# Kernel optimization log

Hardware: AMD Instinct MI355X
Metric: run time of the kernel (lower is better)

Reference implementation:

```python
import jax, jax.numpy as jnp
import numpy as np

N = 100000   # nodes
E = 800000   # edges
D = 128      # uniform hidden width
L = 3        # number of SAGE layers (len(hidden_channels)-1)
EPS = 1e-5   # BatchNorm eps


def setup_inputs() -> dict:
    key = jax.random.key(0)
    ks = jax.random.split(key, 7)
    s = 1.0 / np.sqrt(D)
    x = jax.random.normal(ks[0], (N, D), jnp.float32)
    edge_index = jax.random.randint(ks[1], (2, E), 0, N)
    Wl = jax.random.normal(ks[2], (L, D, D), jnp.float32) * s  # neighbor-branch weight (out,in)
    Wr = jax.random.normal(ks[3], (L, D, D), jnp.float32) * s  # root-branch weight (out,in)
    b = jax.random.normal(ks[4], (L, D), jnp.float32) * 0.01   # bias (lin_l only, PyG default)
    gamma = 1.0 + 0.1 * jax.random.normal(ks[5], (L, D), jnp.float32)
    beta = 0.1 * jax.random.normal(ks[6], (L, D), jnp.float32)
    return {"x": x, "edge_index": edge_index, "Wl": Wl, "Wr": Wr, "b": b,
            "gamma": gamma, "beta": beta}


def _sage(x, src, dst, Wl, Wr, b):
    # PyG SAGEConv: out = lin_l(mean_{j->i} x_j) + lin_r(x_i)
    agg = jax.ops.segment_sum(x[src], dst, num_segments=N)          # [N, D]
    cnt = jax.ops.segment_sum(jnp.ones((src.shape[0], 1), x.dtype), dst,
                              num_segments=N)                        # [N, 1]
    agg = agg / jnp.maximum(cnt, 1.0)  # mean; isolated nodes stay 0
    return agg @ Wl.T + x @ Wr.T + b


def _bn(x, g, be):
    # BatchNorm1d over the node axis, batch statistics, biased variance
    m = jnp.mean(x, axis=0)
    v = jnp.var(x, axis=0)
    return g * (x - m) * jax.lax.rsqrt(v + EPS) + be


def reference(x, edge_index, Wl, Wr, b, gamma, beta):
    src, dst = edge_index[0], edge_index[1]
    # hidden layers: SAGEConv -> ELU -> (dropout, eval no-op) -> BatchNorm
    for i in range(L - 1):
        h = jax.nn.elu(_sage(x, src, dst, Wl[i], Wr[i], b[i]))
        x = _bn(h, gamma[i], beta[i])
    # final layer: SAGEConv -> BatchNorm (no ELU/dropout)
    x = _bn(_sage(x, src, dst, Wl[L - 1], Wr[L - 1], b[L - 1]), gamma[L - 1], beta[L - 1])
    return x
```

## Files before the change

kernel.cpp:

```cpp
#include <hip/hip_runtime.h>
#include <hip/hip_bf16.h>

#define N_NODES 100000
#define N_EDGES 800000
#define DD 128
#define NBLK 1563
#define NSCAN1 391
#define EPSV 1e-5f

typedef short bf16x8 __attribute__((ext_vector_type(8)));
typedef short bf16x4 __attribute__((ext_vector_type(4)));
typedef float f32x4 __attribute__((ext_vector_type(4)));

__device__ __forceinline__ short f2bf(float f) {
    unsigned u = __float_as_uint(f);
    unsigned r = (u + 0x7fffu + ((u >> 16) & 1u)) >> 16;
    return (short)r;
}
__device__ __forceinline__ float bf2f(short s) {
    return __uint_as_float(((unsigned)(unsigned short)s) << 16);
}

__global__ void k_setup(const float* __restrict__ x, short* __restrict__ xbf,
                        const int* __restrict__ dst, int* __restrict__ cnt) {
    int i = blockIdx.x * 256 + threadIdx.x;
    if (i < N_NODES * DD / 8) {
        f32x4 v0 = *(const f32x4*)(x + (size_t)i * 8);
        f32x4 v1 = *(const f32x4*)(x + (size_t)i * 8 + 4);
        bf16x8 t;
        t[0] = f2bf(v0.x); t[1] = f2bf(v0.y); t[2] = f2bf(v0.z); t[3] = f2bf(v0.w);
        t[4] = f2bf(v1.x); t[5] = f2bf(v1.y); t[6] = f2bf(v1.z); t[7] = f2bf(v1.w);
        *(bf16x8*)&xbf[(size_t)i * 8] = t;
    }
    if (i < N_EDGES) atomicAdd(&cnt[dst[i]], 1);
}

__global__ void k_scan1(const int* __restrict__ cnt, int* __restrict__ off,
                        int* __restrict__ bsums) {
    __shared__ int s[256];
    int i = blockIdx.x * 256 + threadIdx.x;
    int t = threadIdx.x;
    s[t] = (i < N_NODES) ? cnt[i] : 0;
    __syncthreads();
    for (int d = 1; d < 256; d <<= 1) {
        int x = 0;
        if (t >= d) x = s[t - d];
        __syncthreads();
        s[t] += x;
        __syncthreads();
    }
    if (i < N_NODES) off[i + 1] = s[t];
    if (t == 255) bsums[blockIdx.x] = s[255];
}

__global__ void k_scan2(int* __restrict__ bsums) {
    __shared__ int s[512];
    int t = threadIdx.x;
    s[t] = (t < NSCAN1) ? bsums[t] : 0;
    __syncthreads();
    for (int d = 1; d < 512; d <<= 1) {
        int x = 0;
        if (t >= d) x = s[t - d];
        __syncthreads();
        s[t] += x;
        __syncthreads();
    }
    if (t < NSCAN1) bsums[t] = s[t];
}

__global__ void k_scan3(int* __restrict__ off, const int* __restrict__ bsums) {
    int i = blockIdx.x * 256 + threadIdx.x;
    int add = (blockIdx.x > 0) ? bsums[blockIdx.x - 1] : 0;
    if (i < N_NODES) off[i + 1] += add;
    if (i == 0) off[0] = 0;
}

__global__ void k_fill(const int* __restrict__ src, const int* __restrict__ dst,
                       const int* __restrict__ off, int* __restrict__ cur,
                       int* __restrict__ elist) {
    int e = blockIdx.x * 256 + threadIdx.x;
    if (e < N_EDGES) {
        int d = dst[e];
        int p = atomicSub(&cur[d], 1);
        elist[off[d] + p - 1] = src[e];
    }
}

__global__ void k_fold(const float* __restrict__ wl, const float* __restrict__ wr,
                       const float* __restrict__ b, const float* __restrict__ aff,
                       int use_aff,
                       short* __restrict__ wblo, short* __restrict__ wbro,
                       float* __restrict__ bias_base, float* __restrict__ bias_deg) {
    int o = blockIdx.x;
    int k = threadIdx.x;
    float a = use_aff ? aff[k] : 1.f;
    float c = use_aff ? aff[128 + k] : 0.f;
    float vl = wl[o * DD + k], vr = wr[o * DD + k];
    wblo[o * DD + k] = f2bf(vl * a);
    wbro[o * DD + k] = f2bf(vr * a);
    __shared__ float s1[128], s2[128];
    s1[k] = c * vr; s2[k] = c * vl;
    __syncthreads();
    for (int d = 64; d > 0; d >>= 1) {
        if (k < d) { s1[k] += s1[k + d]; s2[k] += s2[k + d]; }
        __syncthreads();
    }
    if (k == 0) {
        bias_base[o] = b[o] + s1[0];
        bias_deg[o] = s2[0];
    }
}

template <bool ELU_ON>
__global__ __launch_bounds__(512, 6) void k_sage(
    const short* __restrict__ xbf,
    const int* __restrict__ off, const int* __restrict__ elist,
    const short* __restrict__ wl, const short* __restrict__ wr,
    const float* __restrict__ bias_base, const float* __restrict__ bias_deg,
    short* __restrict__ hout, float* __restrict__ partials)
{
    __shared__ short agg_t[64 * 128];
    __shared__ int sdeg[64];
    __shared__ float sstat[8 * 128];
    const int tid = threadIdx.x;
    const int wu = __builtin_amdgcn_readfirstlane(tid >> 6);
    const int l = tid & 63;
    const int base = blockIdx.x * 64;
    const int qw = l >> 4;
    const int ll = l & 15;

    const int growb = (wu >> 1) * 16 + (wu & 1) * 8;
    for (int i = 0; i < 8; i += 2) {
        const int m0 = growb + i;
        const int m1 = m0 + 1;
        const int g0 = base + m0;
        const int g1 = base + m1;
        float A0[8], A1[8], B0[8], B1[8];
#pragma unroll
        for (int j = 0; j < 8; ++j) { A0[j] = A1[j] = B0[j] = B1[j] = 0.f; }
        int ea = 0, eA = 0, eb = 0, eB = 0;
        if (g0 < N_NODES) { ea = off[g0]; eA = off[g0 + 1]; }
        if (g1 < N_NODES) { eb = off[g1]; eB = off[g1 + 1]; }
        const int dA = eA - ea, dB = eB - eb;
        int e = ea + qw;
        int f = eb + qw;
        while (e + 4 < eA && f + 4 < eB) {
            int s0 = elist[e], s1 = elist[e + 4];
            int s2 = elist[f], s3 = elist[f + 4];
            bf16x8 v0 = *(const bf16x8*)(xbf + (size_t)s0 * DD + 8 * ll);
            bf16x8 v1 = *(const bf16x8*)(xbf + (size_t)s1 * DD + 8 * ll);
            bf16x8 v2 = *(const bf16x8*)(xbf + (size_t)s2 * DD + 8 * ll);
            bf16x8 v3 = *(const bf16x8*)(xbf + (size_t)s3 * DD + 8 * ll);
#pragma unroll
            for (int j = 0; j < 8; ++j) {
                A0[j] += bf2f(v0[j]); A1[j] += bf2f(v1[j]);
                B0[j] += bf2f(v2[j]); B1[j] += bf2f(v3[j]);
            }
            e += 8; f += 8;
        }
        while (e + 4 < eA) {
            int s0 = elist[e], s1 = elist[e + 4];
            bf16x8 v0 = *(const bf16x8*)(xbf + (size_t)s0 * DD + 8 * ll);
            bf16x8 v1 = *(const bf16x8*)(xbf + (size_t)s1 * DD + 8 * ll);
#pragma unroll
            for (int j = 0; j < 8; ++j) { A0[j] += bf2f(v0[j]); A1[j] += bf2f(v1[j]); }
            e += 8;
        }
        if (e < eA) {
            int s0 = elist[e];
            bf16x8 v0 = *(const bf16x8*)(xbf + (size_t)s0 * DD + 8 * ll);
#pragma unroll
            for (int j = 0; j < 8; ++j) A0[j] += bf2f(v0[j]);
        }
        while (f + 4 < eB) {
            int s2 = elist[f], s3 = elist[f + 4];
            bf16x8 v2 = *(const bf16x8*)(xbf + (size_t)s2 * DD + 8 * ll);
            bf16x8 v3 = *(const bf16x8*)(xbf + (size_t)s3 * DD + 8 * ll);
#pragma unroll
            for (int j = 0; j < 8; ++j) { B0[j] += bf2f(v2[j]); B1[j] += bf2f(v3[j]); }
            f += 8;
        }
        if (f < eB) {
            int s2 = elist[f];
            bf16x8 v2 = *(const bf16x8*)(xbf + (size_t)s2 * DD + 8 * ll);
#pragma unroll
            for (int j = 0; j < 8; ++j) B0[j] += bf2f(v2[j]);
        }
#pragma unroll
        for (int j = 0; j < 8; ++j) {
            float sA = A0[j] + A1[j];
            sA += __shfl_xor(sA, 16, 64);
            sA += __shfl_xor(sA, 32, 64);
            A0[j] = sA;
            float sB = B0[j] + B1[j];
            sB += __shfl_xor(sB, 16, 64);
            sB += __shfl_xor(sB, 32, 64);
            B0[j] = sB;
        }
        if (l == 0) { sdeg[m0] = dA; sdeg[m1] = dB; }
        if (qw == 0) {
            float invA = dA > 0 ? 1.f / (float)dA : 0.f;
            float invB = dB > 0 ? 1.f / (float)dB : 0.f;
            bf16x8 tA, tB;
#pragma unroll
            for (int j = 0; j < 8; ++j) { tA[j] = f2bf(A0[j] * invA); tB[j] = f2bf(B0[j] * invB); }
            *(bf16x8*)&agg_t[m0 * DD + ((8 * ll) ^ ((m0 & 7) << 3))] = tA;
            *(bf16x8*)&agg_t[m1 * DD + ((8 * ll) ^ ((m1 & 7) << 3))] = tB;
        }
    }
    __syncthreads();

    const int p = wu >> 1;
    const int half = wu & 1;
    f32x4 acc[4];
#pragma unroll
    for (int nb = 0; nb < 4; ++nb) acc[nb] = f32x4{0.f, 0.f, 0.f, 0.f};
    const int mrow = p * 16 + (l & 15);
    const int kg = (l >> 4) * 8;
    const int nloc = l & 15;
    const int groot = min(base + mrow, N_NODES - 1);
#pragma unroll
    for (int ks = 0; ks < 4; ++ks) {
        int kk = ks * 32 + kg;
        int sw = kk ^ ((mrow & 7) << 3);
        bf16x8 aa = *(const bf16x8*)&agg_t[mrow * DD + sw];
        bf16x8 ax = *(const bf16x8*)(xbf + (size_t)groot * DD + kk);
#pragma unroll
        for (int nb = 0; nb < 4; ++nb) {
            int n = half * 64 + nb * 16 + nloc;
            bf16x8 bl = *(const bf16x8*)&wl[n * DD + kk];
            bf16x8 br = *(const bf16x8*)&wr[n * DD + kk];
            acc[nb] = __builtin_amdgcn_mfma_f32_16x16x32_bf16(aa, bl, acc[nb], 0, 0, 0);
            acc[nb] = __builtin_amdgcn_mfma_f32_16x16x32_bf16(ax, br, acc[nb], 0, 0, 0);
        }
    }
    __syncthreads();

    int degf[4];
#pragma unroll
    for (int r = 0; r < 4; ++r) degf[r] = sdeg[p * 16 + (l >> 4) * 4 + r];

    float colS[4], colQ[4];
#pragma unroll
    for (int nb = 0; nb < 4; ++nb) {
        int n = half * 64 + nb * 16 + nloc;
        float bb = bias_base[n];
        float bd = bias_deg[n];
        float cs = 0.f, cq = 0.f;
#pragma unroll
        for (int r = 0; r < 4; ++r) {
            int m = p * 16 + (l >> 4) * 4 + r;
            int g = base + m;
            float hv = acc[nb][r] + bb + (degf[r] > 0 ? bd : 0.f);
            if (ELU_ON) hv = hv > 0.f ? hv : expm1f(hv);
            agg_t[m * DD + (n ^ ((m & 7) << 3))] = f2bf(hv);
            float hm = (g < N_NODES) ? hv : 0.f;
            cs += hm;
            cq += hm * hm;
        }
        colS[nb] = cs; colQ[nb] = cq;
    }
#pragma unroll
    for (int nb = 0; nb < 4; ++nb) {
        colS[nb] += __shfl_xor(colS[nb], 16, 64);
        colS[nb] += __shfl_xor(colS[nb], 32, 64);
        colQ[nb] += __shfl_xor(colQ[nb], 16, 64);
        colQ[nb] += __shfl_xor(colQ[nb], 32, 64);
    }
    if (l < 16) {
#pragma unroll
        for (int nb = 0; nb < 4; ++nb) {
            sstat[wu * 128 + nb * 16 + l]      = colS[nb];
            sstat[wu * 128 + 64 + nb * 16 + l] = colQ[nb];
        }
    }
    __syncthreads();

#pragma unroll
    for (int k = 0; k < 2; ++k) {
        int idx = (k * 512 + tid) * 8;
        int m = idx >> 7, c = idx & 127;
        int g = base + m;
        if (g < N_NODES) {
            bf16x8 v = *(const bf16x8*)&agg_t[m * DD + (c ^ ((m & 7) << 3))];
            *(bf16x8*)&hout[(size_t)g * DD + c] = v;
        }
    }
    if (tid < 256) {
        int f = tid & 127;
        int part = tid >> 7;
        int hsel = f >> 6;
        int cw = part * 64 + (f & 63);
        float v = 0.f;
#pragma unroll
        for (int pr = 0; pr < 4; ++pr) v += sstat[(2 * pr + hsel) * 128 + cw];
        partials[blockIdx.x * 256 + tid] = v;
    }
}

__global__ void k_reduce(const float* __restrict__ partials,
                         const float* __restrict__ gamma, const float* __restrict__ beta,
                         float* __restrict__ aff) {
    int f = blockIdx.x;
    int t = threadIdx.x;
    float s = 0.f, q = 0.f;
    for (int i = t; i < NBLK; i += 256) {
        s += partials[i * 256 + f];
        q += partials[i * 256 + 128 + f];
    }
    __shared__ float rs[256], rq[256];
    rs[t] = s; rq[t] = q;
    __syncthreads();
    for (int d = 128; d > 0; d >>= 1) {
        if (t < d) { rs[t] += rs[t + d]; rq[t] += rq[t + d]; }
        __syncthreads();
    }
    if (t == 0) {
        float mean = rs[0] / (float)N_NODES;
        float var = rq[0] / (float)N_NODES - mean * mean;
        float a = gamma[f] * rsqrtf(var + EPSV);
        aff[f] = a;
        aff[128 + f] = beta[f] - mean * a;
    }
}

__global__ void k_apply(const short* __restrict__ hin, const float* __restrict__ aff,
                        float* __restrict__ out) {
    int i = blockIdx.x * 256 + threadIdx.x;
    if (i < N_NODES * DD / 8) {
        bf16x8 v = *(const bf16x8*)(hin + (size_t)i * 8);
        int f = (i * 8) & 127;
        f32x4 a0 = *(const f32x4*)(aff + f);
        f32x4 a1 = *(const f32x4*)(aff + f + 4);
        f32x4 c0 = *(const f32x4*)(aff + 128 + f);
        f32x4 c1 = *(const f32x4*)(aff + 128 + f + 4);
        f32x4 o0, o1;
        o0.x = bf2f(v[0]) * a0.x + c0.x; o0.y = bf2f(v[1]) * a0.y + c0.y;
        o0.z = bf2f(v[2]) * a0.z + c0.z; o0.w = bf2f(v[3]) * a0.w + c0.w;
        o1.x = bf2f(v[4]) * a1.x + c1.x; o1.y = bf2f(v[5]) * a1.y + c1.y;
        o1.z = bf2f(v[6]) * a1.z + c1.z; o1.w = bf2f(v[7]) * a1.w + c1.w;
        *(f32x4*)(out + (size_t)i * 8) = o0;
        *(f32x4*)(out + (size_t)i * 8 + 4) = o1;
    }
}

extern "C" void kernel_launch(void* const* d_in, const int* in_sizes, int n_in,
                              void* d_out, int out_size, void* d_ws, size_t ws_size,
                              hipStream_t stream) {
    const float* x     = (const float*)d_in[0];
    const int*   ei    = (const int*)d_in[1];
    const float* Wl    = (const float*)d_in[2];
    const float* Wr    = (const float*)d_in[3];
    const float* b     = (const float*)d_in[4];
    const float* gamma = (const float*)d_in[5];
    const float* beta  = (const float*)d_in[6];
    float* out = (float*)d_out;

    char* ws = (char*)d_ws;
    int*   off      = (int*)(ws + 0);
    int*   cnt      = (int*)(ws + 400128);
    int*   elist    = (int*)(ws + 800256);
    int*   bsums    = (int*)(ws + 4000256);
    float* partials = (float*)(ws + 4002304);
    float* affine   = (float*)(ws + 5603840);
    short* wbl      = (short*)(ws + 5604864);
    short* wbr      = (short*)(ws + 5637632);
    float* biasb    = (float*)(ws + 5670400);
    float* biasd    = (float*)(ws + 5670912);
    short* bufA     = (short*)(ws + 5671424);
    short* bufB     = (short*)(ws + 31271424);

    const int* src = ei;
    const int* dst = ei + N_EDGES;

    hipMemsetAsync(cnt, 0, N_NODES * sizeof(int), stream);
    k_setup<<<(N_NODES * DD / 8 + 255) / 256, 256, 0, stream>>>(x, bufA, dst, cnt);
    k_scan1<<<NSCAN1, 256, 0, stream>>>(cnt, off, bsums);
    k_scan2<<<1, 512, 0, stream>>>(bsums);
    k_scan3<<<NSCAN1, 256, 0, stream>>>(off, bsums);
    k_fill<<<(N_EDGES + 255) / 256, 256, 0, stream>>>(src, dst, off, cnt, elist);

    k_fold<<<128, 128, 0, stream>>>(Wl, Wr, b, affine, 0, wbl, wbr, biasb, biasd);
    k_sage<true><<<NBLK, 512, 0, stream>>>(bufA, off, elist, wbl, wbr,
                                           biasb, biasd, bufB, partials);
    k_reduce<<<128, 256, 0, stream>>>(partials, gamma, beta, affine);

    k_fold<<<128, 128, 0, stream>>>(Wl + DD * DD, Wr + DD * DD, b + DD, affine, 1,
                                    wbl, wbr, biasb, biasd);
    k_sage<true><<<NBLK, 512, 0, stream>>>(bufB, off, elist, wbl, wbr,
                                           biasb, biasd, bufA, partials);
    k_reduce<<<128, 256, 0, stream>>>(partials, gamma + DD, beta + DD, affine);

    k_fold<<<128, 128, 0, stream>>>(Wl + 2 * DD * DD, Wr + 2 * DD * DD, b + 2 * DD,
                                    affine, 1, wbl, wbr, biasb, biasd);
    k_sage<false><<<NBLK, 512, 0, stream>>>(bufA, off, elist, wbl, wbr,
                                            biasb, biasd, bufB, partials);
    k_reduce<<<128, 256, 0, stream>>>(partials, gamma + 2 * DD, beta + 2 * DD, affine);

    k_apply<<<(N_NODES * DD / 8 + 255) / 256, 256, 0, stream>>>(bufB, affine, out);
}
```

Baseline: 430.9 us.

## Stage block edge indices in LDS and balance row pairs via atomic work counter

Each block now loads its 65 CSR offsets and, when they fit, all of its edge source indices into shared memory before aggregation. Row pairs are no longer assigned statically to waves; each wave claims the next pair through an LDS atomic counter to even out load under skewed degrees. This targets index-load latency from global memory and wave imbalance. It costs about 6 KB more LDS and extra barriers, which may lower occupancy under the 512x6 launch bounds, and blocks that exceed the capacity fall back to reading the global edge list.

```diff
diff --git a/kernel.cpp b/kernel.cpp
--- a/kernel.cpp
+++ b/kernel.cpp
@@ -7,6 +7,7 @@
 #define NBLK 1563
 #define NSCAN1 391
 #define EPSV 1e-5f
+#define ECAP 1536
 
 typedef short bf16x8 __attribute__((ext_vector_type(8)));
 typedef short bf16x4 __attribute__((ext_vector_type(4)));
@@ -122,6 +123,9 @@
     __shared__ short agg_t[64 * 128];
     __shared__ int sdeg[64];
     __shared__ float sstat[8 * 128];
+    __shared__ int soff[65];
+    __shared__ int eidx[ECAP];
+    __shared__ int rowctr;
     const int tid = threadIdx.x;
     const int wu = __builtin_amdgcn_readfirstlane(tid >> 6);
     const int l = tid & 63;
@@ -129,24 +133,34 @@
     const int qw = l >> 4;
     const int ll = l & 15;
 
-    const int growb = (wu >> 1) * 16 + (wu & 1) * 8;
-    for (int i = 0; i < 8; i += 2) {
-        const int m0 = growb + i;
+    if (tid < 65) soff[tid] = off[min(base + tid, N_NODES)];
+    if (tid == 0) rowctr = 0;
+    __syncthreads();
+    const int ebase = soff[0];
+    const int etot = soff[64] - ebase;
+    const bool ovf = etot > ECAP;
+    for (int k = tid; k < (ovf ? 0 : etot); k += 512) eidx[k] = elist[ebase + k];
+    __syncthreads();
+    const int* ep = ovf ? (elist + ebase) : (const int*)eidx;
+
+    for (;;) {
+        int rp;
+        if (l == 0) rp = atomicAdd(&rowctr, 1);
+        rp = __shfl(rp, 0, 64);
+        if (rp >= 32) break;
+        const int m0 = rp * 2;
         const int m1 = m0 + 1;
-        const int g0 = base + m0;
-        const int g1 = base + m1;
+        const int ea = soff[m0] - ebase, eA = soff[m0 + 1] - ebase;
+        const int eb = soff[m1] - ebase, eB = soff[m1 + 1] - ebase;
+        const int dA = eA - ea, dB = eB - eb;
         float A0[8], A1[8], B0[8], B1[8];
 #pragma unroll
         for (int j = 0; j < 8; ++j) { A0[j] = A1[j] = B0[j] = B1[j] = 0.f; }
-        int ea = 0, eA = 0, eb = 0, eB = 0;
-        if (g0 < N_NODES) { ea = off[g0]; eA = off[g0 + 1]; }
-        if (g1 < N_NODES) { eb = off[g1]; eB = off[g1 + 1]; }
-        const int dA = eA - ea, dB = eB - eb;
         int e = ea + qw;
         int f = eb + qw;
         while (e + 4 < eA && f + 4 < eB) {
-            int s0 = elist[e], s1 = elist[e + 4];
-            int s2 = elist[f], s3 = elist[f + 4];
+            int s0 = ep[e], s1 = ep[e + 4];
+            int s2 = ep[f], s3 = ep[f + 4];
             bf16x8 v0 = *(const bf16x8*)(xbf + (size_t)s0 * DD + 8 * ll);
             bf16x8 v1 = *(const bf16x8*)(xbf + (size_t)s1 * DD + 8 * ll);
             bf16x8 v2 = *(const bf16x8*)(xbf + (size_t)s2 * DD + 8 * ll);
@@ -159,7 +173,7 @@
             e += 8; f += 8;
         }
         while (e + 4 < eA) {
-            int s0 = elist[e], s1 = elist[e + 4];
+            int s0 = ep[e], s1 = ep[e + 4];
             bf16x8 v0 = *(const bf16x8*)(xbf + (size_t)s0 * DD + 8 * ll);
             bf16x8 v1 = *(const bf16x8*)(xbf + (size_t)s1 * DD + 8 * ll);
 #pragma unroll
@@ -167,13 +181,13 @@
             e += 8;
         }
         if (e < eA) {
-            int s0 = elist[e];
+            int s0 = ep[e];
             bf16x8 v0 = *(const bf16x8*)(xbf + (size_t)s0 * DD + 8 * ll);
 #pragma unroll
             for (int j = 0; j < 8; ++j) A0[j] += bf2f(v0[j]);
         }
         while (f + 4 < eB) {
-            int s2 = elist[f], s3 = elist[f + 4];
+            int s2 = ep[f], s3 = ep[f + 4];
             bf16x8 v2 = *(const bf16x8*)(xbf + (size_t)s2 * DD + 8 * ll);
             bf16x8 v3 = *(const bf16x8*)(xbf + (size_t)s3 * DD + 8 * ll);
 #pragma unroll
@@ -181,7 +195,7 @@
             f += 8;
         }
         if (f < eB) {
-            int s2 = elist[f];
+            int s2 = ep[f];
             bf16x8 v2 = *(const bf16x8*)(xbf + (size_t)s2 * DD + 8 * ll);
 #pragma unroll
             for (int j = 0; j < 8; ++j) B0[j] += bf2f(v2[j]);
```

Measured after the change: 418.5 us. 1.03x faster.

## Shrink SAGE tile to 32 nodes, stage edge lists in LDS, one-node-per-quarter-wave gather

Applied to the files above, without the earlier changes.

The fused SAGE kernel now processes 32 nodes per 256-thread block instead of 64 per 512, doubling the block count. Each block stages its contiguous edge-index range into shared memory, falling back to global memory if the range overflows. The gather now assigns one node to each 16-lane quarter-wave, with a two-deep software-pipelined prefetch loop, which removes the cross-quarter shuffle reduction. The aim is better load balance and more memory parallelism, at the cost of divergence from uneven degrees within a wave and twice as many partial-statistic rows for the reduction.

```diff
diff --git a/kernel.cpp b/kernel.cpp
--- a/kernel.cpp
+++ b/kernel.cpp
@@ -4,12 +4,13 @@
 #define N_NODES 100000
 #define N_EDGES 800000
 #define DD 128
-#define NBLK 1563
+#define TILE 32
+#define NBLK 3125
 #define NSCAN1 391
 #define EPSV 1e-5f
+#define ECAP 768
 
 typedef short bf16x8 __attribute__((ext_vector_type(8)));
-typedef short bf16x4 __attribute__((ext_vector_type(4)));
 typedef float f32x4 __attribute__((ext_vector_type(4)));
 
 __device__ __forceinline__ short f2bf(float f) {
@@ -112,101 +113,72 @@
 }
 
 template <bool ELU_ON>
-__global__ __launch_bounds__(512, 6) void k_sage(
+__global__ __launch_bounds__(256, 6) void k_sage(
     const short* __restrict__ xbf,
     const int* __restrict__ off, const int* __restrict__ elist,
     const short* __restrict__ wl, const short* __restrict__ wr,
     const float* __restrict__ bias_base, const float* __restrict__ bias_deg,
     short* __restrict__ hout, float* __restrict__ partials)
 {
-    __shared__ short agg_t[64 * 128];
-    __shared__ int sdeg[64];
-    __shared__ float sstat[8 * 128];
+    __shared__ short agg_t[TILE * 128];
+    __shared__ int sdeg[TILE];
+    __shared__ float sstat[4 * 128];
+    __shared__ int soff[TILE + 1];
+    __shared__ int eidx[ECAP];
     const int tid = threadIdx.x;
     const int wu = __builtin_amdgcn_readfirstlane(tid >> 6);
     const int l = tid & 63;
-    const int base = blockIdx.x * 64;
+    const int base = blockIdx.x * TILE;
     const int qw = l >> 4;
     const int ll = l & 15;
 
-    const int growb = (wu >> 1) * 16 + (wu & 1) * 8;
-    for (int i = 0; i < 8; i += 2) {
-        const int m0 = growb + i;
-        const int m1 = m0 + 1;
-        const int g0 = base + m0;
-        const int g1 = base + m1;
-        float A0[8], A1[8], B0[8], B1[8];
-#pragma unroll
-        for (int j = 0; j < 8; ++j) { A0[j] = A1[j] = B0[j] = B1[j] = 0.f; }
-        int ea = 0, eA = 0, eb = 0, eB = 0;
-        if (g0 < N_NODES) { ea = off[g0]; eA = off[g0 + 1]; }
-        if (g1 < N_NODES) { eb = off[g1]; eB = off[g1 + 1]; }
-        const int dA = eA - ea, dB = eB - eb;
-        int e = ea + qw;
-        int f = eb + qw;
-        while (e + 4 < eA && f + 4 < eB) {
-            int s0 = elist[e], s1 = elist[e + 4];
-            int s2 = elist[f], s3 = elist[f + 4];
-            bf16x8 v0 = *(const bf16x8*)(xbf + (size_t)s0 * DD + 8 * ll);
-            bf16x8 v1 = *(const bf16x8*)(xbf + (size_t)s1 * DD + 8 * ll);
-            bf16x8 v2 = *(const bf16x8*)(xbf + (size_t)s2 * DD + 8 * ll);
-            bf16x8 v3 = *(const bf16x8*)(xbf + (size_t)s3 * DD + 8 * ll);
-#pragma unroll
-            for (int j = 0; j < 8; ++j) {
-                A0[j] += bf2f(v0[j]); A1[j] += bf2f(v1[j]);
-                B0[j] += bf2f(v2[j]); B1[j] += bf2f(v3[j]);
+    if (tid < TILE + 1) soff[tid] = off[min(base + tid, N_NODES)];
+    __syncthreads();
+    const int ebase = soff[0];
+    const int etot = soff[TILE] - ebase;
+    const bool ovf = etot > ECAP;
+    for (int k = tid; k < (ovf ? 0 : etot); k += 256) eidx[k] = elist[ebase + k];
+    __syncthreads();
+    const int* ep = ovf ? (elist + ebase) : (const int*)eidx;
+
+#pragma unroll
+    for (int q = 0; q < 2; ++q) {
+        const int m = wu * 8 + q * 4 + qw;
+        const int ea = soff[m] - ebase;
+        const int eA = soff[m + 1] - ebase;
+        const int deg = eA - ea;
+        float acc[8];
+#pragma unroll
+        for (int j = 0; j < 8; ++j) acc[j] = 0.f;
+
+        int e = ea;
+        bool val0 = e < eA, val1 = e + 1 < eA;
+        bf16x8 v0{}, v1{};
+        if (val0) v0 = *(const bf16x8*)(xbf + (size_t)ep[e] * DD + 8 * ll);
+        if (val1) v1 = *(const bf16x8*)(xbf + (size_t)ep[e + 1] * DD + 8 * ll);
+        while (__any((int)(val0 || val1))) {
+            int en = e + 2;
+            bool nv0 = en < eA, nv1 = en + 1 < eA;
+            bf16x8 w0{}, w1{};
+            if (nv0) w0 = *(const bf16x8*)(xbf + (size_t)ep[en] * DD + 8 * ll);
+            if (nv1) w1 = *(const bf16x8*)(xbf + (size_t)ep[en + 1] * DD + 8 * ll);
+            if (val0) {
+#pragma unroll
+                for (int j = 0; j < 8; ++j) acc[j] += bf2f(v0[j]);
             }
-            e += 8; f += 8;
-        }
-        while (e + 4 < eA) {
-            int s0 = elist[e], s1 = elist[e + 4];
-            bf16x8 v0 = *(const bf16x8*)(xbf + (size_t)s0 * DD + 8 * ll);
-            bf16x8 v1 = *(const bf16x8*)(xbf + (size_t)s1 * DD + 8 * ll);
-#pragma unroll
-            for (int j = 0; j < 8; ++j) { A0[j] += bf2f(v0[j]); A1[j] += bf2f(v1[j]); }
-            e += 8;
-        }
-        if (e < eA) {
-            int s0 = elist[e];
-            bf16x8 v0 = *(const bf16x8*)(xbf + (size_t)s0 * DD + 8 * ll);
-#pragma unroll
-            for (int j = 0; j < 8; ++j) A0[j] += bf2f(v0[j]);
-        }
-        while (f + 4 < eB) {
-            int s2 = elist[f], s3 = elist[f + 4];
-            bf16x8 v2 = *(const bf16x8*)(xbf + (size_t)s2 * DD + 8 * ll);
-            bf16x8 v3 = *(const bf16x8*)(xbf + (size_t)s3 * DD + 8 * ll);
-#pragma unroll
-            for (int j = 0; j < 8; ++j) { B0[j] += bf2f(v2[j]); B1[j] += bf2f(v3[j]); }
-            f += 8;
-        }
-        if (f < eB) {
-            int s2 = elist[f];
-            bf16x8 v2 = *(const bf16x8*)(xbf + (size_t)s2 * DD + 8 * ll);
-#pragma unroll
-            for (int j = 0; j < 8; ++j) B0[j] += bf2f(v2[j]);
-        }
-#pragma unroll
-        for (int j = 0; j < 8; ++j) {
-            float sA = A0[j] + A1[j];
-            sA += __shfl_xor(sA, 16, 64);
-            sA += __shfl_xor(sA, 32, 64);
-            A0[j] = sA;
-            float sB = B0[j] + B1[j];
-            sB += __shfl_xor(sB, 16, 64);
-            sB += __shfl_xor(sB, 32, 64);
-            B0[j] = sB;
-        }
-        if (l == 0) { sdeg[m0] = dA; sdeg[m1] = dB; }
-        if (qw == 0) {
-            float invA = dA > 0 ? 1.f / (float)dA : 0.f;
-            float invB = dB > 0 ? 1.f / (float)dB : 0.f;
-            bf16x8 tA, tB;
-#pragma unroll
-            for (int j = 0; j < 8; ++j) { tA[j] = f2bf(A0[j] * invA); tB[j] = f2bf(B0[j] * invB); }
-            *(bf16x8*)&agg_t[m0 * DD + ((8 * ll) ^ ((m0 & 7) << 3))] = tA;
-            *(bf16x8*)&agg_t[m1 * DD + ((8 * ll) ^ ((m1 & 7) << 3))] = tB;
-        }
+            if (val1) {
+#pragma unroll
+                for (int j = 0; j < 8; ++j) acc[j] += bf2f(v1[j]);
+            }
+            v0 = w0; v1 = w1; val0 = nv0; val1 = nv1; e = en;
+        }
+
+        float inv = deg > 0 ? 1.f / (float)deg : 0.f;
+        bf16x8 t;
+#pragma unroll
+        for (int j = 0; j < 8; ++j) t[j] = f2bf(acc[j] * inv);
+        *(bf16x8*)&agg_t[m * DD + ((8 * ll) ^ ((m & 7) << 3))] = t;
+        if (ll == 0) sdeg[m] = deg;
     }
     __syncthreads();
 
@@ -278,7 +250,7 @@
 
 #pragma unroll
     for (int k = 0; k < 2; ++k) {
-        int idx = (k * 512 + tid) * 8;
+        int idx = (k * 256 + tid) * 8;
         int m = idx >> 7, c = idx & 127;
         int g = base + m;
         if (g < N_NODES) {
@@ -286,14 +258,14 @@
             *(bf16x8*)&hout[(size_t)g * DD + c] = v;
         }
     }
-    if (tid < 256) {
+    {
         int f = tid & 127;
         int part = tid >> 7;
         int hsel = f >> 6;
         int cw = part * 64 + (f & 63);
         float v = 0.f;
 #pragma unroll
-        for (int pr = 0; pr < 4; ++pr) v += sstat[(2 * pr + hsel) * 128 + cw];
+        for (int pr = 0; pr < 2; ++pr) v += sstat[(2 * pr + hsel) * 128 + cw];
         partials[blockIdx.x * 256 + tid] = v;
     }
 }
@@ -362,13 +334,13 @@
     int*   elist    = (int*)(ws + 800256);
     int*   bsums    = (int*)(ws + 4000256);
     float* partials = (float*)(ws + 4002304);
-    float* affine   = (float*)(ws + 5603840);
-    short* wbl      = (short*)(ws + 5604864);
-    short* wbr      = (short*)(ws + 5637632);
-    float* biasb    = (float*)(ws + 5670400);
-    float* biasd    = (float*)(ws + 5670912);
-    short* bufA     = (short*)(ws + 5671424);
-    short* bufB     = (short*)(ws + 31271424);
+    float* affine   = (float*)(ws + 7202304);
+    short* wbl      = (short*)(ws + 7203328);
+    short* wbr      = (short*)(ws + 7236096);
+    float* biasb    = (float*)(ws + 7268864);
+    float* biasd    = (float*)(ws + 7269376);
+    short* bufA     = (short*)(ws + 7269888);
+    short* bufB     = (short*)(ws + 32869888);
 
     const int* src = ei;
     const int* dst = ei + N_EDGES;
@@ -381,19 +353,19 @@
     k_fill<<<(N_EDGES + 255) / 256, 256, 0, stream>>>(src, dst, off, cnt, elist);
 
     k_fold<<<128, 128, 0, stream>>>(Wl, Wr, b, affine, 0, wbl, wbr, biasb, biasd);
-    k_sage<true><<<NBLK, 512, 0, stream>>>(bufA, off, elist, wbl, wbr,
+    k_sage<true><<<NBLK, 256, 0, stream>>>(bufA, off, elist, wbl, wbr,
                                            biasb, biasd, bufB, partials);
     k_reduce<<<128, 256, 0, stream>>>(partials, gamma, beta, affine);
 
     k_fold<<<128, 128, 0, stream>>>(Wl + DD * DD, Wr + DD * DD, b + DD, affine, 1,
                                     wbl, wbr, biasb, biasd);
-    k_sage<true><<<NBLK, 512, 0, stream>>>(bufB, off, elist, wbl, wbr,
+    k_sage<true><<<NBLK, 256, 0, stream>>>(bufB, off, elist, wbl, wbr,
                                            biasb, biasd, bufA, partials);
     k_reduce<<<128, 256, 0, stream>>>(partials, gamma + DD, beta + DD, affine);
 
     k_fold<<<128, 128, 0, stream>>>(Wl + 2 * DD * DD, Wr + 2 * DD * DD, b + 2 * DD,
                                     affine, 1, wbl, wbr, biasb, biasd);
-    k_sage<false><<<NBLK, 512, 0, stream>>>(bufA, off, elist, wbl, wbr,
+    k_sage<false><<<NBLK, 256, 0, stream>>>(bufA, off, elist, wbl, wbr,
                                             biasb, biasd, bufB, partials);
     k_reduce<<<128, 256, 0, stream>>>(partials, gamma + 2 * DD, beta + 2 * DD, affine);
 
```

Result: faster. 408.2 us (-5.3%).
